# Optimization experiments

Measured on AMD Instinct MI355X. Metric: run time of the kernel, lower is better.

The kernel has to match this reference:

```python
import jax, jax.numpy as jnp
import numpy as np

B, T, D, H = 2, 2048, 1024, 16
DK = D // H
NEG = -1e9  # stand-in for -inf; causal mask guarantees >=1 valid key per row


def setup_inputs() -> dict:
    key = jax.random.key(0)
    ks = jax.random.split(key, 9)
    s = 1.0 / np.sqrt(D)
    x = jax.random.normal(ks[0], (B, T, D), dtype=jnp.float32)
    mask = jnp.broadcast_to(jnp.tril(jnp.ones((T, T), dtype=jnp.int32))[None, None], (B, 1, T, T))
    params = {}
    for i, n in enumerate(['q', 'k', 'v', 'o']):
        params['W' + n] = jax.random.normal(ks[1 + 2 * i], (D, D), dtype=jnp.float32) * s
        params['b' + n] = jax.random.normal(ks[2 + 2 * i], (D,), dtype=jnp.float32) * s
    return dict(x=x, mask=mask, **params)


def reference(x, mask, Wq, bq, Wk, bk, Wv, bv, Wo, bo):
    Bx, Tx, Dx = x.shape
    # projections: [B,T,D] -> [B,H,T,DK]
    def split_heads(y):
        return y.reshape(Bx, Tx, H, DK).transpose(0, 2, 1, 3)
    Q = split_heads(x @ Wq + bq)
    K = split_heads(x @ Wk + bk)
    V = split_heads(x @ Wv + bv)
    scores = jnp.einsum('bhqd,bhkd->bhqk', Q, K) / jnp.sqrt(jnp.float32(DK))
    scores = jnp.where(mask == 0, NEG, scores)
    attn = jax.nn.softmax(scores, axis=-1)  # dropout is identity in eval / p=0
    out = jnp.einsum('bhqk,bhkd->bhqd', attn, V)
    out = out.transpose(0, 2, 1, 3).reshape(Bx, Tx, Dx)
    return out @ Wo + bo
```

## Files before the change

### kernel.cpp

```cpp
#include <hip/hip_runtime.h>
#include <hip/hip_bf16.h>

typedef __bf16 bf16;
typedef __attribute__((ext_vector_type(8))) __bf16 bf16x8;
typedef __attribute__((ext_vector_type(4))) __bf16 bf16x4;
typedef __attribute__((ext_vector_type(4))) float f32x4;
typedef __attribute__((ext_vector_type(16))) float f32x16;
typedef __attribute__((ext_vector_type(4))) int int4v;

#define TSEQ 2048
#define DMODEL 1024
#define NHEAD 16
#define DKH 64
#define BATCH 2
#define NQKV 3072

typedef __attribute__((address_space(1))) const void gv_t;
typedef __attribute__((address_space(3))) void sv_t;
__device__ __forceinline__ void gll16(const bf16* g, bf16* s) {
    __builtin_amdgcn_global_load_lds((gv_t*)g, (sv_t*)s, 16, 0, 0);
}
#define WAIT_VM(n) __builtin_amdgcn_s_waitcnt(0x0F70 | (n))

__device__ __forceinline__ unsigned cvtpk(float lo, float hi) {
    unsigned d;
    asm("v_cvt_pk_bf16_f32 %0, %1, %2" : "=v"(d) : "v"(lo), "v"(hi));
    return d;
}

#define PREP_CONV 4096
#define PREP_TW   4096
#define PREP_GRID (PREP_CONV + PREP_TW + 12)
__global__ __launch_bounds__(256) void prep(
    const float* __restrict__ x,
    const float* __restrict__ Wq, const float* __restrict__ Wk,
    const float* __restrict__ Wv, const float* __restrict__ Wo,
    const float* __restrict__ bq, const float* __restrict__ bk,
    const float* __restrict__ bv,
    bf16* __restrict__ xb, bf16* __restrict__ WT, float* __restrict__ biasO)
{
    __shared__ float t[32][33];
    int bid = blockIdx.x;
    const int tid = threadIdx.x;
    if (bid < PREP_CONV) {
        int i = (bid * 256 + tid) * 4;
        f32x4 v = *(const f32x4*)(x + i);
        bf16x4 o;
#pragma unroll
        for (int j = 0; j < 4; ++j) o[j] = (bf16)v[j];
        *(bf16x4*)(xb + i) = o;
        return;
    }
    bid -= PREP_CONV;
    if (bid < PREP_TW) {
        int z = bid >> 10;
        int by = ((bid >> 5) & 31) * 32, bx = (bid & 31) * 32;
        const float* W = z == 0 ? Wq : z == 1 ? Wk : z == 2 ? Wv : Wo;
        bf16* T = WT + (size_t)z * DMODEL * DMODEL;
        int tx = tid & 31, ty = tid >> 5;
#pragma unroll
        for (int i = 0; i < 4; ++i)
            t[ty + i * 8][tx] = W[(size_t)(by + ty + i * 8) * DMODEL + bx + tx];
        __syncthreads();
#pragma unroll
        for (int i = 0; i < 4; ++i)
            T[(size_t)(bx + ty + i * 8) * DMODEL + by + tx] = (bf16)t[tx][ty + i * 8];
        return;
    }
    bid -= PREP_TW;
    int i = bid * 256 + tid;
    float v = i < 1024 ? bq[i] : i < 2048 ? bk[i - 1024] : bv[i - 2048];
    biasO[i] = v;
}

template <typename OutT, int NW_N, bool FUSE_VT>
__global__ __launch_bounds__(256) void gemm_bias_kernel(
    const bf16* __restrict__ A, const bf16* __restrict__ BT,
    const float* __restrict__ bias, OutT* __restrict__ C, int ldc,
    bf16* __restrict__ VT)
{
    constexpr int BN    = NW_N * 64;
    constexpr int MW    = 4 / NW_N;
    constexpr int WROWS = 128 / MW;
    constexpr int FM    = WROWS / 16;
    constexpr int ASZ   = 128 * 32;
    constexpr int BSZ   = BN * 32;
    constexpr int BNP   = BN + 4;
    constexpr int TST   = 136;
    constexpr int EPI   = sizeof(OutT) == 2 ? (FUSE_VT ? 128 * TST : 128 * BN)
                                            : 64 * BNP * 2;
    constexpr int STG   = 3 * ASZ + 3 * BSZ;
    constexpr int SMEM  = STG > EPI ? STG : EPI;
    __shared__ bf16 smem[SMEM];
    bf16* As0 = smem;
    bf16* Bs0 = smem + 3 * ASZ;

    const int tid = threadIdx.x;
    const int ln = tid & 63, wave = tid >> 6;
    const int wm = NW_N == 2 ? (wave >> 1) : wave;
    const int wn = NW_N == 2 ? (wave & 1) : 0;
    const int lr = ln & 15, quad = ln >> 4;
    const int m0 = blockIdx.y * 128, n0 = blockIdx.x * BN;

    f32x4 acc[FM][4] = {};

    const int grow = ln >> 2;
    const int gcol = (ln & 3) * 8;
    const bf16* Ag = A + (size_t)(m0 + wave * 32 + grow) * DMODEL + gcol;
    const bf16* Bg = BT + (size_t)(n0 + (NW_N == 2 ? wave * 32 : wave * 16) + grow) * DMODEL + gcol;

    auto stage = [&](int buf, int kk) {
        bf16* AsW = As0 + buf * ASZ + wave * 1024;
        gll16(Ag + kk, AsW);
        gll16(Ag + (size_t)16 * DMODEL + kk, AsW + 512);
        if constexpr (NW_N == 2) {
            bf16* BsW = Bs0 + buf * BSZ + wave * 1024;
            gll16(Bg + kk, BsW);
            gll16(Bg + (size_t)16 * DMODEL + kk, BsW + 512);
        } else {
            gll16(Bg + kk, Bs0 + buf * BSZ + wave * 512);
        }
    };

    constexpr int NT = DMODEL / 32;
    stage(0, 0);
    stage(1, 32);
    for (int kt = 0, cur = 0; kt < NT; ++kt, cur = cur == 2 ? 0 : cur + 1) {
        if (kt + 1 < NT) { if constexpr (NW_N == 2) WAIT_VM(4); else WAIT_VM(3); }
        else WAIT_VM(0);
        __syncthreads();
        if (kt + 2 < NT) stage(cur == 0 ? 2 : cur - 1, (kt + 2) * 32);
        const bf16* AsB = As0 + cur * ASZ;
        const bf16* BsB = Bs0 + cur * BSZ;
        bf16x8 af[FM], bfr[4];
#pragma unroll
        for (int i = 0; i < FM; ++i)
            af[i] = *(const bf16x8*)(AsB + (wm * WROWS + i * 16 + lr) * 32 + quad * 8);
#pragma unroll
        for (int j = 0; j < 4; ++j)
            bfr[j] = *(const bf16x8*)(BsB + (wn * 64 + j * 16 + lr) * 32 + quad * 8);
#pragma unroll
        for (int i = 0; i < FM; ++i)
#pragma unroll
            for (int j = 0; j < 4; ++j)
                acc[i][j] = __builtin_amdgcn_mfma_f32_16x16x32_bf16(
                    af[i], bfr[j], acc[i][j], 0, 0, 0);
    }
    __syncthreads();

    if constexpr (sizeof(OutT) == 2) {
        if (FUSE_VT && n0 >= 2048) {
            bf16* Cs = smem;
#pragma unroll
            for (int j = 0; j < 4; ++j) {
                int nl = wn * 64 + j * 16 + lr;
                float bv = bias[n0 + nl];
#pragma unroll
                for (int i = 0; i < FM; ++i) {
                    int ml = wm * WROWS + i * 16 + quad * 4;
#pragma unroll
                    for (int r = 0; r < 4; ++r)
                        Cs[nl * TST + ml + r] = (bf16)(acc[i][j][r] + bv);
                }
            }
            __syncthreads();
            const int bb = m0 >> 11;
            const int tloc = m0 & 2047;
#pragma unroll
            for (int pp = 0; pp < 8; ++pp) {
                int dl = pp * 16 + (tid >> 4);
                int t0 = (tid & 15) * 8;
                bf16x8 v = *(const bf16x8*)(Cs + dl * TST + t0);
                *(bf16x8*)(VT + (size_t)(bb * 1024 + (n0 - 2048) + dl) * TSEQ +
                           tloc + t0) = v;
            }
            return;
        }
        bf16* Cs = smem;
#pragma unroll
        for (int j = 0; j < 4; ++j) {
            int nl = wn * 64 + j * 16 + lr;
            float bv = bias[n0 + nl];
#pragma unroll
            for (int i = 0; i < FM; ++i) {
                int ml = wm * WROWS + i * 16 + quad * 4;
#pragma unroll
                for (int r = 0; r < 4; ++r)
                    Cs[(ml + r) * BN + nl] = (bf16)(acc[i][j][r] + bv);
            }
        }
        __syncthreads();
        constexpr int LPR = BN / 8;
        constexpr int RPP = 256 / LPR;
        const int rr = tid / LPR, cc = (tid % LPR) * 8;
#pragma unroll
        for (int pp = 0; pp < 128 / RPP; ++pp) {
            int row = pp * RPP + rr;
            *(bf16x8*)(C + (size_t)(m0 + row) * ldc + n0 + cc) =
                *(const bf16x8*)(Cs + row * BN + cc);
        }
    } else {
        float* Cf = (float*)smem;
#pragma unroll
        for (int half = 0; half < 2; ++half) {
            if (((wm * WROWS) >> 6) == half) {
#pragma unroll
                for (int j = 0; j < 4; ++j) {
                    int nl = wn * 64 + j * 16 + lr;
                    float bv = bias[n0 + nl];
#pragma unroll
                    for (int i = 0; i < FM; ++i) {
                        int ml = wm * WROWS + i * 16 + quad * 4 - half * 64;
#pragma unroll
                        for (int r = 0; r < 4; ++r)
                            Cf[(ml + r) * BNP + nl] = acc[i][j][r] + bv;
                    }
                }
            }
            __syncthreads();
            constexpr int LPR = BN / 4;
            constexpr int RPP = 256 / LPR;
            const int rr = tid / LPR, cc = (tid % LPR) * 4;
#pragma unroll
            for (int pp = 0; pp < 64 / RPP; ++pp) {
                int row = pp * RPP + rr;
                *(f32x4*)(C + (size_t)(m0 + half * 64 + row) * ldc + n0 + cc) =
                    *(const f32x4*)(Cf + row * BNP + cc);
            }
            __syncthreads();
        }
    }
}

template <int KTN, bool MASKED>
__device__ __forceinline__ void tile_step(
    int kt0, int kc, int qabs,
    const bf16* __restrict__ Ksb, const bf16* __restrict__ Vsb,
    const bf16x8 qf[4], f32x16 oacc[2], float& lrow,
    int ln31, int hi, int sw)
{
    f32x16 st[KTN] = {};
    __builtin_amdgcn_s_setprio(1);
#pragma unroll
    for (int t = 0; t < KTN; ++t)
#pragma unroll
        for (int ks = 0; ks < 4; ++ks) {
            const bf16x8 ka = *(const bf16x8*)(
                Ksb + (ln31 + (kt0 + t) * 32) * 64 + (((2 * ks + hi) ^ sw) * 8));
            st[t] = __builtin_amdgcn_mfma_f32_32x32x16_bf16(ka, qf[ks], st[t], 0, 0, 0);
        }
    __builtin_amdgcn_s_setprio(0);

    const float scale2 = 0.18033688f;
    float rs = 0.f;
#pragma unroll
    for (int t = 0; t < KTN; ++t)
#pragma unroll
        for (int r = 0; r < 16; ++r) {
            float p = exp2f(fmaf(st[t][r], scale2, -24.0f));
            if (MASKED &&
                (kc + (kt0 + t) * 32 + (r & 3) + 8 * (r >> 2) + 4 * hi > qabs))
                p = 0.f;
            rs += p;
            st[t][r] = p;
        }
    rs += __shfl_xor(rs, 32);
    lrow += rs;

    __builtin_amdgcn_s_setprio(1);
#pragma unroll
    for (int t = 0; t < KTN; ++t)
#pragma unroll
        for (int s2 = 0; s2 < 2; ++s2) {
            const int bb = s2 * 8;
            unsigned c01 = cvtpk(st[t][bb + 0], st[t][bb + 1]);
            unsigned c23 = cvtpk(st[t][bb + 2], st[t][bb + 3]);
            unsigned c45 = cvtpk(st[t][bb + 4], st[t][bb + 5]);
            unsigned c67 = cvtpk(st[t][bb + 6], st[t][bb + 7]);
            asm("v_permlane32_swap_b32 %0, %1" : "+v"(c01), "+v"(c45));
            asm("v_permlane32_swap_b32 %0, %1" : "+v"(c23), "+v"(c67));
            int4v pw;
            pw[0] = (int)c01; pw[1] = (int)c23; pw[2] = (int)c45; pw[3] = (int)c67;
            const bf16x8 pa = __builtin_bit_cast(bf16x8, pw);
            const int ksg = (kt0 + t) * 2 + s2;
#pragma unroll
            for (int dblk = 0; dblk < 2; ++dblk) {
                const bf16x8 vb = *(const bf16x8*)(
                    Vsb + (dblk * 32 + ln31) * 64 + (((2 * ksg + hi) ^ sw) * 8));
                oacc[dblk] = __builtin_amdgcn_mfma_f32_32x32x16_bf16(
                    pa, vb, oacc[dblk], 0, 0, 0);
            }
        }
    __builtin_amdgcn_s_setprio(0);
}

__global__ __launch_bounds__(256, 2) void flash_attn(
    const bf16* __restrict__ QKV, const bf16* __restrict__ VT,
    bf16* __restrict__ O)
{
    __shared__ bf16 Ks[4][64 * 64];
    __shared__ bf16 Vs[4][64 * 64];
    const int tid = threadIdx.x;
    const int ln = tid & 63, w = tid >> 6;
    const int ln31 = ln & 31, hi = ln >> 5, sw = ln & 7;
    const int wg = blockIdx.x;
    const int g = wg & 31, p = wg >> 5;
    const int h = g >> 1, b = g & 1;
    const int q0A = p * 64, q0B = (31 - p) * 64;

    const bf16* Qb = QKV + (size_t)b * TSEQ * NQKV + h * DKH;
    const bf16* Kb = Qb + 1024;
    const bf16* VTb = VT + (size_t)(b * NHEAD + h) * DKH * TSEQ;

    const int q1 = (w < 2 ? q0A : q0B) + (w & 1) * 32 + ln31;
    const int q2 = q0B + (w & 1) * 32 + ln31;

    bf16x8 qf1[4], qf2[4];
#pragma unroll
    for (int ks = 0; ks < 4; ++ks) {
        qf1[ks] = *(const bf16x8*)(Qb + (size_t)q1 * NQKV + ks * 16 + hi * 8);
        qf2[ks] = *(const bf16x8*)(Qb + (size_t)q2 * NQKV + ks * 16 + hi * 8);
    }
    WAIT_VM(0);

    const int srow = (w & 1) * 32 + (ln >> 3);
    const int scol = ((ln & 7) ^ ((ln >> 3) & 7)) * 8;
    const bool stK = (w < 2);
    auto stage = [&](int buf, int kc) {
        if (stK) {
            const bf16* g2 = Kb + (size_t)(kc + srow) * NQKV + scol;
            bf16* s = &Ks[buf][(w & 1) * 32 * 64];
#pragma unroll
            for (int l = 0; l < 4; ++l)
                gll16(g2 + (size_t)(l * 8) * NQKV, s + l * 8 * 64);
        } else {
            const bf16* g2 = VTb + (size_t)srow * TSEQ + kc + scol;
            bf16* s = &Vs[buf][(w & 1) * 32 * 64];
#pragma unroll
            for (int l = 0; l < 4; ++l)
                gll16(g2 + (size_t)(l * 8) * TSEQ, s + l * 8 * 64);
        }
    };

    f32x16 oacc1[2] = {}, oacc2[2] = {};
    float l1 = 0.f, l2 = 0.f;

    const int nld = 32 - p;

    auto do_chunk = [&](int c) {
        const int kc = c * 64;
        const bf16* K = Ks[c & 3];
        const bf16* V = Vs[c & 3];
        if (c <= p) {
            if (w < 2 && c == p)
                tile_step<2, true >(0, kc, q1, K, V, qf1, oacc1, l1, ln31, hi, sw);
            else
                tile_step<2, false>(0, kc, q1, K, V, qf1, oacc1, l1, ln31, hi, sw);
        } else {
            const int kt0 = w >> 1;
            if (c == nld - 1)
                tile_step<1, true >(kt0, kc, q2, K, V, qf2, oacc2, l2, ln31, hi, sw);
            else
                tile_step<1, false>(kt0, kc, q2, K, V, qf2, oacc2, l2, ln31, hi, sw);
        }
    };

    stage(0, 0);
    stage(1, 64);
    for (int c = 0; c < nld; c += 2) {
        WAIT_VM(0);
        __syncthreads();
        if (c + 2 < nld) stage((c + 2) & 3, (c + 2) * 64);
        if (c + 3 < nld) stage((c + 3) & 3, (c + 3) * 64);
        do_chunk(c);
        if (c + 1 < nld) do_chunk(c + 1);
    }
    __syncthreads();

    float* exO = (float*)&Ks[0][0];
    float* exL = (float*)&Vs[0][0];
    if (w < 2) {
        float* dst = exO + w * 2048;
#pragma unroll
        for (int dblk = 0; dblk < 2; ++dblk)
#pragma unroll
            for (int r = 0; r < 16; ++r) {
                int q = (r & 3) + 8 * (r >> 2) + 4 * hi;
                dst[q * 64 + dblk * 32 + ln31] = oacc2[dblk][r];
            }
        if (ln < 32) exL[w * 32 + ln] = l2;
    }
    __syncthreads();

    f32x16 oat[2];
    float lt;
    int qs;
    if (w < 2) {
        oat[0] = oacc1[0]; oat[1] = oacc1[1];
        lt = l1;
        qs = q0A + (w & 1) * 32;
    } else {
        const float* src = exO + (w - 2) * 2048;
        lt = l1 + l2 + exL[(w - 2) * 32 + ln31];
#pragma unroll
        for (int dblk = 0; dblk < 2; ++dblk)
#pragma unroll
            for (int r = 0; r < 16; ++r) {
                int q = (r & 3) + 8 * (r >> 2) + 4 * hi;
                oat[dblk][r] = oacc1[dblk][r] + oacc2[dblk][r] +
                               src[q * 64 + dblk * 32 + ln31];
            }
        qs = q0B + (w & 1) * 32;
    }

#pragma unroll
    for (int r = 0; r < 16; ++r) {
        const int crow = (r & 3) + 8 * (r >> 2) + 4 * hi;
        const float inv = 1.0f / __shfl(lt, crow);
        const int row = qs + crow;
#pragma unroll
        for (int dblk = 0; dblk < 2; ++dblk)
            O[(size_t)(b * TSEQ + row) * DMODEL + h * DKH + dblk * 32 + ln31] =
                (bf16)(oat[dblk][r] * inv);
    }
}

extern "C" void kernel_launch(void* const* d_in, const int* in_sizes, int n_in,
                              void* d_out, int out_size, void* d_ws, size_t ws_size,
                              hipStream_t stream)
{
    const float* x  = (const float*)d_in[0];
    const float* Wq = (const float*)d_in[2];
    const float* bq = (const float*)d_in[3];
    const float* Wk = (const float*)d_in[4];
    const float* bk = (const float*)d_in[5];
    const float* Wv = (const float*)d_in[6];
    const float* bv = (const float*)d_in[7];
    const float* Wo = (const float*)d_in[8];
    const float* bo = (const float*)d_in[9];

    char* ws = (char*)d_ws;
    bf16* xb   = (bf16*)(ws);
    bf16* QKV  = (bf16*)(ws + (8u  << 20));
    bf16* VT   = (bf16*)(ws + (32u << 20));
    bf16* O    = (bf16*)(ws + (40u << 20));
    bf16* WT   = (bf16*)(ws + (48u << 20));
    float* wsBias = (float*)O;

    prep<<<PREP_GRID, 256, 0, stream>>>(x, Wq, Wk, Wv, Wo, bq, bk, bv,
                                        xb, WT, wsBias);

    gemm_bias_kernel<bf16, 2, true><<<dim3(NQKV / 128, 32), 256, 0, stream>>>(
        xb, WT, wsBias, QKV, NQKV, VT);

    flash_attn<<<512, 256, 0, stream>>>(QKV, VT, O);

    gemm_bias_kernel<float, 1, false><<<dim3(DMODEL / 64, 32), 256, 0, stream>>>(
        O, WT + 3u * (1u << 20), bo, (float*)d_out, DMODEL, nullptr);
}
```

Before: 201.2 us.

## Use BK=64 double-buffered GEMM with XOR-swizzled LDS and XCD-aware block remap

Doubles the GEMM K-tile to 64 and switches from a 3-stage to a 2-stage LDS pipeline, so there are half as many barriers per K loop. An XOR swizzle is applied to the LDS column layout to avoid bank conflicts on the wider rows. A 1D grid with a remap that assigns contiguous chunks of tiles to each of the 8 XCDs is meant to improve L2 reuse. Waiting for all loads at the end of each iteration shortens the prefetch distance, which may expose more memory latency.

```diff
diff --git a/kernel.cpp b/kernel.cpp
--- a/kernel.cpp
+++ b/kernel.cpp
@@ -83,70 +83,86 @@
     constexpr int MW    = 4 / NW_N;
     constexpr int WROWS = 128 / MW;
     constexpr int FM    = WROWS / 16;
-    constexpr int ASZ   = 128 * 32;
-    constexpr int BSZ   = BN * 32;
+    constexpr int BK    = 64;
+    constexpr int ASZ   = 128 * BK;
+    constexpr int BSZ   = BN * BK;
     constexpr int BNP   = BN + 4;
     constexpr int TST   = 136;
     constexpr int EPI   = sizeof(OutT) == 2 ? (FUSE_VT ? 128 * TST : 128 * BN)
                                             : 64 * BNP * 2;
-    constexpr int STG   = 3 * ASZ + 3 * BSZ;
+    constexpr int STG   = 2 * ASZ + 2 * BSZ;
     constexpr int SMEM  = STG > EPI ? STG : EPI;
     __shared__ bf16 smem[SMEM];
     bf16* As0 = smem;
-    bf16* Bs0 = smem + 3 * ASZ;
+    bf16* Bs0 = smem + 2 * ASZ;
 
     const int tid = threadIdx.x;
     const int ln = tid & 63, wave = tid >> 6;
     const int wm = NW_N == 2 ? (wave >> 1) : wave;
     const int wn = NW_N == 2 ? (wave & 1) : 0;
     const int lr = ln & 15, quad = ln >> 4;
-    const int m0 = blockIdx.y * 128, n0 = blockIdx.x * BN;
+
+    constexpr int NBX = (NW_N == 2) ? 24 : 16;
+    constexpr int CH  = (NW_N == 2) ? 96 : 64;
+    const int wg  = blockIdx.x;
+    const int lin = (wg & 7) * CH + (wg >> 3);
+    const int m0  = (lin / NBX) * 128, n0 = (lin % NBX) * BN;
 
     f32x4 acc[FM][4] = {};
 
-    const int grow = ln >> 2;
-    const int gcol = (ln & 3) * 8;
-    const bf16* Ag = A + (size_t)(m0 + wave * 32 + grow) * DMODEL + gcol;
-    const bf16* Bg = BT + (size_t)(n0 + (NW_N == 2 ? wave * 32 : wave * 16) + grow) * DMODEL + gcol;
+    const int srow = ln >> 3;
+    const int scol = ((ln & 7) ^ srow) * 8;
+    const bf16* Ag = A + (size_t)(m0 + wave * 32 + srow) * DMODEL + scol;
+    const bf16* Bg = BT + (size_t)(n0 + (NW_N == 2 ? wave * 32 : wave * 16) + srow) * DMODEL + scol;
 
     auto stage = [&](int buf, int kk) {
-        bf16* AsW = As0 + buf * ASZ + wave * 1024;
-        gll16(Ag + kk, AsW);
-        gll16(Ag + (size_t)16 * DMODEL + kk, AsW + 512);
+        bf16* AsW = As0 + buf * ASZ + wave * (32 * BK);
+#pragma unroll
+        for (int l = 0; l < 4; ++l)
+            gll16(Ag + (size_t)(l * 8) * DMODEL + kk, AsW + l * 8 * BK);
         if constexpr (NW_N == 2) {
-            bf16* BsW = Bs0 + buf * BSZ + wave * 1024;
-            gll16(Bg + kk, BsW);
-            gll16(Bg + (size_t)16 * DMODEL + kk, BsW + 512);
+            bf16* BsW = Bs0 + buf * BSZ + wave * (32 * BK);
+#pragma unroll
+            for (int l = 0; l < 4; ++l)
+                gll16(Bg + (size_t)(l * 8) * DMODEL + kk, BsW + l * 8 * BK);
         } else {
-            gll16(Bg + kk, Bs0 + buf * BSZ + wave * 512);
+            bf16* BsW = Bs0 + buf * BSZ + wave * (16 * BK);
+#pragma unroll
+            for (int l = 0; l < 2; ++l)
+                gll16(Bg + (size_t)(l * 8) * DMODEL + kk, BsW + l * 8 * BK);
         }
     };
 
-    constexpr int NT = DMODEL / 32;
+    constexpr int NT = DMODEL / BK;
     stage(0, 0);
-    stage(1, 32);
-    for (int kt = 0, cur = 0; kt < NT; ++kt, cur = cur == 2 ? 0 : cur + 1) {
-        if (kt + 1 < NT) { if constexpr (NW_N == 2) WAIT_VM(4); else WAIT_VM(3); }
-        else WAIT_VM(0);
+    WAIT_VM(0);
+    __syncthreads();
+    const int swr = lr & 7;
+    for (int kt = 0; kt < NT; ++kt) {
+        if (kt + 1 < NT) stage((kt + 1) & 1, (kt + 1) * BK);
+        const bf16* AsB = As0 + (kt & 1) * ASZ;
+        const bf16* BsB = Bs0 + (kt & 1) * BSZ;
+#pragma unroll
+        for (int k2 = 0; k2 < 2; ++k2) {
+            bf16x8 af[FM], bfr[4];
+#pragma unroll
+            for (int i = 0; i < FM; ++i)
+                af[i] = *(const bf16x8*)(AsB + (wm * WROWS + i * 16 + lr) * BK +
+                                         (((k2 * 4 + quad) ^ swr) * 8));
+#pragma unroll
+            for (int j = 0; j < 4; ++j)
+                bfr[j] = *(const bf16x8*)(BsB + (wn * 64 + j * 16 + lr) * BK +
+                                          (((k2 * 4 + quad) ^ swr) * 8));
+#pragma unroll
+            for (int i = 0; i < FM; ++i)
+#pragma unroll
+                for (int j = 0; j < 4; ++j)
+                    acc[i][j] = __builtin_amdgcn_mfma_f32_16x16x32_bf16(
+                        af[i], bfr[j], acc[i][j], 0, 0, 0);
+        }
+        WAIT_VM(0);
         __syncthreads();
-        if (kt + 2 < NT) stage(cur == 0 ? 2 : cur - 1, (kt + 2) * 32);
-        const bf16* AsB = As0 + cur * ASZ;
-        const bf16* BsB = Bs0 + cur * BSZ;
-        bf16x8 af[FM], bfr[4];
-#pragma unroll
-        for (int i = 0; i < FM; ++i)
-            af[i] = *(const bf16x8*)(AsB + (wm * WROWS + i * 16 + lr) * 32 + quad * 8);
-#pragma unroll
-        for (int j = 0; j < 4; ++j)
-            bfr[j] = *(const bf16x8*)(BsB + (wn * 64 + j * 16 + lr) * 32 + quad * 8);
-#pragma unroll
-        for (int i = 0; i < FM; ++i)
-#pragma unroll
-            for (int j = 0; j < 4; ++j)
-                acc[i][j] = __builtin_amdgcn_mfma_f32_16x16x32_bf16(
-                    af[i], bfr[j], acc[i][j], 0, 0, 0);
-    }
-    __syncthreads();
+    }
 
     if constexpr (sizeof(OutT) == 2) {
         if (FUSE_VT && n0 >= 2048) {
@@ -450,11 +466,11 @@
     prep<<<PREP_GRID, 256, 0, stream>>>(x, Wq, Wk, Wv, Wo, bq, bk, bv,
                                         xb, WT, wsBias);
 
-    gemm_bias_kernel<bf16, 2, true><<<dim3(NQKV / 128, 32), 256, 0, stream>>>(
+    gemm_bias_kernel<bf16, 2, true><<<768, 256, 0, stream>>>(
         xb, WT, wsBias, QKV, NQKV, VT);
 
     flash_attn<<<512, 256, 0, stream>>>(QKV, VT, O);
 
-    gemm_bias_kernel<float, 1, false><<<dim3(DMODEL / 64, 32), 256, 0, stream>>>(
+    gemm_bias_kernel<float, 1, false><<<512, 256, 0, stream>>>(
         O, WT + 3u * (1u << 20), bo, (float*)d_out, DMODEL, nullptr);
 }
```

Result: no change. 198.7 us, median of 3 (-1.2%).
